# Kernel tuning notes

Hardware: AMD Instinct MI355X
Metric: run time of the kernel (lower is better)

Reference implementation:

```python
import jax, jax.numpy as jnp
import numpy as np

B_SZ, C_IN, C_OUT, H, W = 16, 32, 32, 128, 128
K, CODE, PAD, FACTOR = 3, 2, 1, 1.0

def setup_inputs() -> dict:
    key = jax.random.key(0)
    ks = jax.random.split(key, 7)
    s = 0.05
    return {
        "x": jax.random.normal(ks[0], (B_SZ, C_IN, H, W), jnp.float32),
        "codes": jax.random.normal(ks[1], (B_SZ, CODE, CODE), jnp.float32),
        "weight": jax.random.normal(ks[2], (C_OUT, C_IN, K, K), jnp.float32) * s,
        "A": jax.random.normal(ks[3], (C_IN, CODE, K, K), jnp.float32) * s,
        "Bm": jax.random.normal(ks[4], (C_OUT, CODE, K, K), jnp.float32) * s,
        "bias": jax.random.normal(ks[5], (C_OUT,), jnp.float32) * s,
        "bias_context": jax.random.normal(ks[6], (CODE, C_OUT), jnp.float32) * s,
    }

def reference(x, codes, weight, A, Bm, bias, bias_context):
    # hypernetwork weight synthesis: [b, out, in, k, k]
    w_ctx = jnp.einsum('ickl,bcr->birkl', A, codes)            # [b, in, code, k, k]
    w_ctx = jnp.einsum('birkl,orkl->boikl', w_ctx, Bm)         # [b, out, in, k, k]
    combined_weight = weight[None] + FACTOR * w_ctx
    # per-sample bias from diagonal of codes
    diag = jnp.diagonal(codes, axis1=-2, axis2=-1)             # [b, code]
    combined_bias = bias[None] + FACTOR * (diag @ bias_context)  # [b, out]
    # circular padding then per-sample VALID conv (== unfold + einsum)
    xp = jnp.pad(x, ((0, 0), (0, 0), (PAD, PAD), (PAD, PAD)), mode='wrap')
    def conv_one(xi, wi):
        return jax.lax.conv_general_dilated(
            xi[None], wi, window_strides=(1, 1), padding='VALID',
            dimension_numbers=('NCHW', 'OIHW', 'NCHW'))[0]
    out = jax.vmap(conv_one)(xp, combined_weight)              # [b, out, H, W]
    return out + combined_bias[:, :, None, None]
```

## Files before the change

kernel.cpp:

```cpp
#include <hip/hip_runtime.h>

typedef short bf16x8 __attribute__((ext_vector_type(8)));
typedef float f32x4  __attribute__((ext_vector_type(4)));
typedef unsigned short u16;
typedef unsigned int   u32;

#define HH 128
#define WW 128

__device__ __forceinline__ u32 cvt_pk_bf16(float lo, float hi) {
    u32 r;
    asm volatile("v_cvt_pk_bf16_f32 %0, %1, %2" : "=v"(r) : "v"(lo), "v"(hi));
    return r;
}

__global__ __launch_bounds__(512, 1) void geps_mfma_kernel(
    const float* __restrict__ x, const float* __restrict__ codes,
    const float* __restrict__ weight, const float* __restrict__ A,
    const float* __restrict__ Bm, const float* __restrict__ bias,
    const float* __restrict__ bctx, float* __restrict__ out)
{
    __shared__ bf16x8 lds_x[3072];
    __shared__ bf16x8 lds_w[1152];
    __shared__ float  lds_ctx[576];
    __shared__ float  lds_b[32];

    const int tid  = threadIdx.x;
    const int l    = tid & 63;
    const int wvid = tid >> 6;
    const int row  = wvid >> 1;
    const int oh   = wvid & 1;

    const int orig = blockIdx.x;
    const int vb   = (orig & 7) * 32 + (orig >> 3);
    const int b    = vb >> 4;
    const int pair = vb & 15;
    const int h0   = pair * 4;
    const int h1   = h0 + 64;

    const float c00 = codes[b * 4 + 0];
    const float c01 = codes[b * 4 + 1];
    const float c10 = codes[b * 4 + 2];
    const float c11 = codes[b * 4 + 3];

    for (int j = tid; j < 576; j += 512) {
        int i = j / 18, rem = j % 18, r = rem / 9, kl = rem % 9;
        float a0 = A[(i * 2 + 0) * 9 + kl];
        float a1 = A[(i * 2 + 1) * 9 + kl];
        lds_ctx[j] = (r == 0) ? (a0 * c00 + a1 * c10) : (a0 * c01 + a1 * c11);
    }
    if (tid < 32) lds_b[tid] = bias[tid] + c00 * bctx[tid] + c11 * bctx[32 + tid];
    __syncthreads();

    for (int j = tid; j < 1152; j += 512) {
        int kl = j >> 7, rem = j & 127, o = rem >> 2, kb = rem & 3;
        float m0 = Bm[(o * 2 + 0) * 9 + kl];
        float m1 = Bm[(o * 2 + 1) * 9 + kl];
        float wf[8];
        #pragma unroll
        for (int jj = 0; jj < 8; ++jj) {
            int i = kb * 8 + jj;
            wf[jj] = weight[(o * 32 + i) * 9 + kl]
                   + lds_ctx[i * 18 + kl] * m0
                   + lds_ctx[i * 18 + 9 + kl] * m1;
        }
        u32 pk[4];
        #pragma unroll
        for (int q = 0; q < 4; ++q) pk[q] = cvt_pk_bf16(wf[2 * q], wf[2 * q + 1]);
        *(uint4*)&lds_w[kl * 128 + (o >> 4) * 64 + kb * 16 + (o & 15)] =
            make_uint4(pk[0], pk[1], pk[2], pk[3]);
    }

    #pragma unroll
    for (int it = 0; it < 3; ++it) {
        int idx = it * 512 + tid;
        int cp  = idx & 63;
        int ig  = (idx >> 6) & 3;
        int rr  = idx >> 8;
        int c0  = cp * 2;
        int grow = (h0 - 1 + rr) & 127;
        const float* src = x + ((size_t)(b * 32 + ig * 8) * HH + grow) * WW + c0;
        float2 f[8];
        #pragma unroll
        for (int jj = 0; jj < 8; ++jj)
            f[jj] = *(const float2*)(src + (size_t)jj * HH * WW);
        u32 p0[4], p1[4];
        #pragma unroll
        for (int q = 0; q < 4; ++q) {
            p0[q] = cvt_pk_bf16(f[2 * q].x, f[2 * q + 1].x);
            p1[q] = cvt_pk_bf16(f[2 * q].y, f[2 * q + 1].y);
        }
        int didx = rr * 512 + (c0 >> 4) * 64 + ig * 16 + (c0 & 15);
        *(uint4*)&lds_x[didx]     = make_uint4(p0[0], p0[1], p0[2], p0[3]);
        *(uint4*)&lds_x[didx + 1] = make_uint4(p1[0], p1[1], p1[2], p1[3]);
    }
    __syncthreads();

    const int awb = oh * 64 + (l >> 4) * 16 + (l & 15);
    bf16x8 af[9];
    #pragma unroll
    for (int kl = 0; kl < 9; ++kl)
        af[kl] = lds_w[kl * 128 + awb];

    const int p = l & 15, igf = l >> 4;
    int bb[3];
    #pragma unroll
    for (int dl = -1; dl <= 1; ++dl) {
        int pq = p + dl;
        bb[dl + 1] = (pq & 15) + ((pq >> 4) << 6) + igf * 16;
    }

    float blr[4];
    #pragma unroll
    for (int r = 0; r < 4; ++r) blr[r] = lds_b[oh * 16 + (l >> 4) * 4 + r];

    auto compute_store = [&](int hbase) {
        f32x4 acc[8];
        #pragma unroll
        for (int nt = 0; nt < 8; ++nt) acc[nt] = (f32x4){0.f, 0.f, 0.f, 0.f};
        #pragma unroll
        for (int nt = 0; nt < 8; ++nt) {
            #pragma unroll
            for (int lc = 0; lc < 3; ++lc) {
                int t = (bb[lc] + nt * 64) & 511;
                #pragma unroll
                for (int k = 0; k < 3; ++k) {
                    bf16x8 bfv = lds_x[(row + k) * 512 + t];
                    acc[nt] = __builtin_amdgcn_mfma_f32_16x16x32_bf16(
                        af[k * 3 + lc], bfv, acc[nt], 0, 0, 0);
                }
            }
        }
        const int h = hbase + row;
        const size_t obase =
            ((size_t)(b * 32 + oh * 16 + (l >> 4) * 4) * HH + h) * WW + p;
        #pragma unroll
        for (int nt = 0; nt < 8; ++nt)
            #pragma unroll
            for (int r = 0; r < 4; ++r)
                out[obase + (size_t)r * (HH * WW) + nt * 16] = acc[nt][r] + blr[r];
    };

    float2 pf[24];
    #pragma unroll
    for (int it = 0; it < 3; ++it) {
        int idx = it * 512 + tid;
        int cp  = idx & 63;
        int ig  = (idx >> 6) & 3;
        int rr  = idx >> 8;
        int grow = (h1 - 1 + rr) & 127;
        const float* src = x + ((size_t)(b * 32 + ig * 8) * HH + grow) * WW + cp * 2;
        #pragma unroll
        for (int jj = 0; jj < 8; ++jj)
            pf[it * 8 + jj] = *(const float2*)(src + (size_t)jj * HH * WW);
    }

    compute_store(h0);

    __syncthreads();

    #pragma unroll
    for (int it = 0; it < 3; ++it) {
        int idx = it * 512 + tid;
        int cp  = idx & 63;
        int ig  = (idx >> 6) & 3;
        int rr  = idx >> 8;
        int c0  = cp * 2;
        u32 p0[4], p1[4];
        #pragma unroll
        for (int q = 0; q < 4; ++q) {
            p0[q] = cvt_pk_bf16(pf[it * 8 + 2 * q].x, pf[it * 8 + 2 * q + 1].x);
            p1[q] = cvt_pk_bf16(pf[it * 8 + 2 * q].y, pf[it * 8 + 2 * q + 1].y);
        }
        int didx = rr * 512 + (c0 >> 4) * 64 + ig * 16 + (c0 & 15);
        *(uint4*)&lds_x[didx]     = make_uint4(p0[0], p0[1], p0[2], p0[3]);
        *(uint4*)&lds_x[didx + 1] = make_uint4(p1[0], p1[1], p1[2], p1[3]);
    }
    __syncthreads();

    compute_store(h1);
}

extern "C" void kernel_launch(void* const* d_in, const int* in_sizes, int n_in,
                              void* d_out, int out_size, void* d_ws, size_t ws_size,
                              hipStream_t stream) {
    const float* x      = (const float*)d_in[0];
    const float* codes  = (const float*)d_in[1];
    const float* weight = (const float*)d_in[2];
    const float* A      = (const float*)d_in[3];
    const float* Bm     = (const float*)d_in[4];
    const float* bias   = (const float*)d_in[5];
    const float* bctx   = (const float*)d_in[6];
    float* out = (float*)d_out;

    hipLaunchKernelGGL(geps_mfma_kernel, dim3(256), dim3(512), 0, stream,
                       x, codes, weight, A, Bm, bias, bctx, out);
}
```

Baseline: 24.49 us.

## Process 8 contiguous rows per block with ring-buffered halo reuse

Each block now handles 8 consecutive output rows instead of two separate 4-row groups. The second phase keeps two halo rows already in LDS in a ring buffer and loads only 4 new rows, which cuts global reads of x. Waves are also regrouped so each wave covers both output-channel halves over half the columns. Every B fragment read from LDS now feeds two MFMAs, halving LDS reads per MFMA, at the cost of holding twice as many weight fragments and accumulators in registers.

Result: faster. 23.54 us (-3.9%).

```diff
diff --git a/kernel.cpp b/kernel.cpp
--- a/kernel.cpp
+++ b/kernel.cpp
@@ -29,14 +29,13 @@
     const int l    = tid & 63;
     const int wvid = tid >> 6;
     const int row  = wvid >> 1;
-    const int oh   = wvid & 1;
+    const int nh   = wvid & 1;
 
     const int orig = blockIdx.x;
     const int vb   = (orig & 7) * 32 + (orig >> 3);
     const int b    = vb >> 4;
-    const int pair = vb & 15;
-    const int h0   = pair * 4;
-    const int h1   = h0 + 64;
+    const int grp  = vb & 15;
+    const int h0   = grp * 8;
 
     const float c00 = codes[b * 4 + 0];
     const float c01 = codes[b * 4 + 1];
@@ -96,11 +95,13 @@
     }
     __syncthreads();
 
-    const int awb = oh * 64 + (l >> 4) * 16 + (l & 15);
-    bf16x8 af[9];
+    const int awb = (l >> 4) * 16 + (l & 15);
+    bf16x8 af[9][2];
     #pragma unroll
     for (int kl = 0; kl < 9; ++kl)
-        af[kl] = lds_w[kl * 128 + awb];
+        #pragma unroll
+        for (int oh = 0; oh < 2; ++oh)
+            af[kl][oh] = lds_w[kl * 128 + oh * 64 + awb];
 
     const int p = l & 15, igf = l >> 4;
     int bb[3];
@@ -110,57 +111,68 @@
         bb[dl + 1] = (pq & 15) + ((pq >> 4) << 6) + igf * 16;
     }
 
-    float blr[4];
-    #pragma unroll
-    for (int r = 0; r < 4; ++r) blr[r] = lds_b[oh * 16 + (l >> 4) * 4 + r];
-
-    auto compute_store = [&](int hbase) {
-        f32x4 acc[8];
-        #pragma unroll
-        for (int nt = 0; nt < 8; ++nt) acc[nt] = (f32x4){0.f, 0.f, 0.f, 0.f};
-        #pragma unroll
-        for (int nt = 0; nt < 8; ++nt) {
+    float blr[2][4];
+    #pragma unroll
+    for (int oh = 0; oh < 2; ++oh)
+        #pragma unroll
+        for (int r = 0; r < 4; ++r)
+            blr[oh][r] = lds_b[oh * 16 + (l >> 4) * 4 + r];
+
+    auto compute_store = [&](int s0, int s1, int s2, int h) {
+        f32x4 acc[2][4];
+        #pragma unroll
+        for (int oh = 0; oh < 2; ++oh)
+            #pragma unroll
+            for (int q = 0; q < 4; ++q) acc[oh][q] = (f32x4){0.f, 0.f, 0.f, 0.f};
+        const int sl[3] = {s0, s1, s2};
+        #pragma unroll
+        for (int q = 0; q < 4; ++q) {
+            const int nt = nh * 4 + q;
             #pragma unroll
             for (int lc = 0; lc < 3; ++lc) {
                 int t = (bb[lc] + nt * 64) & 511;
                 #pragma unroll
                 for (int k = 0; k < 3; ++k) {
-                    bf16x8 bfv = lds_x[(row + k) * 512 + t];
-                    acc[nt] = __builtin_amdgcn_mfma_f32_16x16x32_bf16(
-                        af[k * 3 + lc], bfv, acc[nt], 0, 0, 0);
+                    bf16x8 bfv = lds_x[sl[k] * 512 + t];
+                    acc[0][q] = __builtin_amdgcn_mfma_f32_16x16x32_bf16(
+                        af[k * 3 + lc][0], bfv, acc[0][q], 0, 0, 0);
+                    acc[1][q] = __builtin_amdgcn_mfma_f32_16x16x32_bf16(
+                        af[k * 3 + lc][1], bfv, acc[1][q], 0, 0, 0);
                 }
             }
         }
-        const int h = hbase + row;
         const size_t obase =
-            ((size_t)(b * 32 + oh * 16 + (l >> 4) * 4) * HH + h) * WW + p;
-        #pragma unroll
-        for (int nt = 0; nt < 8; ++nt)
+            ((size_t)(b * 32 + (l >> 4) * 4) * HH + h) * WW + p;
+        #pragma unroll
+        for (int oh = 0; oh < 2; ++oh)
             #pragma unroll
-            for (int r = 0; r < 4; ++r)
-                out[obase + (size_t)r * (HH * WW) + nt * 16] = acc[nt][r] + blr[r];
+            for (int q = 0; q < 4; ++q)
+                #pragma unroll
+                for (int r = 0; r < 4; ++r)
+                    out[obase + (size_t)(oh * 16 + r) * (HH * WW) + (nh * 4 + q) * 16] =
+                        acc[oh][q][r] + blr[oh][r];
     };
 
-    float2 pf[24];
-    #pragma unroll
-    for (int it = 0; it < 3; ++it) {
+    float2 pf[16];
+    #pragma unroll
+    for (int it = 0; it < 2; ++it) {
         int idx = it * 512 + tid;
         int cp  = idx & 63;
         int ig  = (idx >> 6) & 3;
         int rr  = idx >> 8;
-        int grow = (h1 - 1 + rr) & 127;
+        int grow = (h0 + 5 + rr) & 127;
         const float* src = x + ((size_t)(b * 32 + ig * 8) * HH + grow) * WW + cp * 2;
         #pragma unroll
         for (int jj = 0; jj < 8; ++jj)
             pf[it * 8 + jj] = *(const float2*)(src + (size_t)jj * HH * WW);
     }
 
-    compute_store(h0);
-
-    __syncthreads();
-
-    #pragma unroll
-    for (int it = 0; it < 3; ++it) {
+    compute_store(row, row + 1, row + 2, h0 + row);
+
+    __syncthreads();
+
+    #pragma unroll
+    for (int it = 0; it < 2; ++it) {
         int idx = it * 512 + tid;
         int cp  = idx & 63;
         int ig  = (idx >> 6) & 3;
@@ -178,7 +190,13 @@
     }
     __syncthreads();
 
-    compute_store(h1);
+    {
+        int r0 = 4 + row, r1 = 5 + row, r2 = 6 + row;
+        compute_store(r0 >= 6 ? r0 - 6 : r0,
+                      r1 >= 6 ? r1 - 6 : r1,
+                      r2 >= 6 ? r2 - 6 : r2,
+                      h0 + 4 + row);
+    }
 }
 
 extern "C" void kernel_launch(void* const* d_in, const int* in_sizes, int n_in,
```
